# Kernel tuning notes

Hardware: AMD Instinct MI355X
Metric: run time of the kernel (lower is better)

The kernel has to match this reference:

```python
import jax, jax.numpy as jnp
import numpy as np

N_NODES = 50000
N_EDGES = 800000
IN_DIM = 128
HID_DIM = 128
OUT_DIM = 128


def setup_inputs() -> dict:
    key = jax.random.key(0)
    k = jax.random.split(key, 8)
    x = jax.random.normal(k[0], (N_NODES, IN_DIM), dtype=jnp.float32)
    edge_index = jax.random.randint(k[1], (2, N_EDGES), 0, N_NODES, dtype=jnp.int64)
    edge_weight = jax.random.uniform(k[2], (N_EDGES,), dtype=jnp.float32)
    # GCNConv params: weight [in, out] (glorot-ish), bias [out]
    W1 = jax.random.normal(k[3], (IN_DIM, HID_DIM), dtype=jnp.float32) / np.sqrt(IN_DIM)
    b1 = jnp.zeros((HID_DIM,), dtype=jnp.float32)
    W2 = jax.random.normal(k[4], (HID_DIM, OUT_DIM), dtype=jnp.float32) / np.sqrt(HID_DIM)
    b2 = jnp.zeros((OUT_DIM,), dtype=jnp.float32)
    return {"x": x, "edge_index": edge_index, "edge_weight": edge_weight,
            "W1": W1, "b1": b1, "W2": W2, "b2": b2}


def gcn_conv(x, W, b, src, dst, ew, n_nodes):
    """PyG GCNConv: add self-loops (weight 1), symmetric D^-1/2 (A+I) D^-1/2 norm."""
    h = x @ W  # [N, out]
    deg = jax.ops.segment_sum(ew, dst, num_segments=n_nodes) + 1.0  # +1 for self loop
    dis = jnp.where(deg > 0, jax.lax.rsqrt(deg), 0.0)  # deg^{-1/2}
    norm = dis[src] * ew * dis[dst]  # [E]
    msg = h[src] * norm[:, None]  # gather + weight -> [E, out]
    agg = jax.ops.segment_sum(msg, dst, num_segments=n_nodes)
    # self-loop contribution: norm_ii = dis[i] * 1 * dis[i]
    agg = agg + h * (dis * dis)[:, None]
    return agg + b


def reference(x, edge_index, edge_weight, W1, b1, W2, b2):
    src, dst = edge_index[0], edge_index[1]
    n = x.shape[0]
    h = gcn_conv(x, W1, b1, src, dst, edge_weight, n)
    h = jax.nn.relu(h)
    out = gcn_conv(h, W2, b2, src, dst, edge_weight, n)
    return out
```

## Files before the change

kernel.cpp:

```cpp
#include <hip/hip_runtime.h>

#define NDIM 128
#define NPART 8

typedef __attribute__((ext_vector_type(8))) short bf16x8;
typedef __attribute__((ext_vector_type(4))) float floatx4;

__device__ __forceinline__ float bflo(unsigned v){ return __uint_as_float(v << 16); }
__device__ __forceinline__ float bfhi(unsigned v){ return __uint_as_float(v & 0xffff0000u); }
__device__ __forceinline__ unsigned f2bf(float f){
  unsigned u = __float_as_uint(f);
  return (u + 0x7fffu + ((u >> 16) & 1u)) >> 16;
}

__global__ void k_prep0(unsigned long long* __restrict__ pk,
                        const float* __restrict__ W1, const float* __restrict__ W2,
                        unsigned short* __restrict__ Wp1, unsigned short* __restrict__ Wp2,
                        int n){
  int i = blockIdx.x * 256 + threadIdx.x;
  if (i < n) pk[i] = 0ULL;
  if (i < NDIM * NDIM){
    int k = i >> 7, c = i & 127;
    int kt = k >> 5, kq = (k >> 3) & 3, j = k & 7;
    int Lb = kq * 16 + (c & 15);
    int idx = (((kt * 8 + (c >> 4)) * 64) + Lb) * 8 + j;
    Wp1[idx] = (unsigned short)f2bf(W1[i]);
    Wp2[idx] = (unsigned short)f2bf(W2[i]);
  }
}

__global__ void k_deg(const int* __restrict__ ei, const float* __restrict__ ew,
                      unsigned long long* pk, unsigned short* __restrict__ rank, int E){
  int e = blockIdx.x * blockDim.x + threadIdx.x;
  if (e >= E) return;
  int d = ei[E + e];
  unsigned fx = (unsigned)__float2uint_rn(ew[e] * 1048576.0f);
  unsigned long long old = atomicAdd(&pk[d], (1ULL << 44) | (unsigned long long)fx);
  rank[e] = (unsigned short)(old >> 44);
}

__global__ __launch_bounds__(1024) void k_scan1(const unsigned long long* __restrict__ pk,
                                                int* __restrict__ off,
                                                int* __restrict__ bsum, int n){
  __shared__ int wsum[16];
  int t = threadIdx.x;
  int i = blockIdx.x * 1024 + t;
  int c = (i < n) ? (int)(pk[i] >> 44) : 0;
  int lane = t & 63, w = t >> 6;
  int v = c;
  #pragma unroll
  for (int d = 1; d < 64; d <<= 1){ int u = __shfl_up(v, d); if (lane >= d) v += u; }
  if (lane == 63) wsum[w] = v;
  __syncthreads();
  if (w == 0){
    int sv = (lane < 16) ? wsum[lane] : 0;
    #pragma unroll
    for (int d = 1; d < 16; d <<= 1){ int u = __shfl_up(sv, d); if (lane >= d) sv += u; }
    if (lane < 16) wsum[lane] = sv;
  }
  __syncthreads();
  int base = (w > 0) ? wsum[w - 1] : 0;
  if (i < n) off[i] = base + v - c;
  if (t == 1023) bsum[blockIdx.x] = wsum[15];
}

__global__ __launch_bounds__(1024) void k_scan23(int* __restrict__ off,
                                                 const int* __restrict__ bsum,
                                                 const unsigned long long* __restrict__ pk,
                                                 float* __restrict__ dis, int n, int E, int nb){
  __shared__ int sBase;
  int t = threadIdx.x;
  if (t < 64){
    int c2 = (t < nb) ? bsum[t] : 0;
    int v2 = c2;
    #pragma unroll
    for (int d = 1; d < 64; d <<= 1){ int u = __shfl_up(v2, d); if (t >= d) v2 += u; }
    if (t == (int)blockIdx.x) sBase = v2 - c2;
  }
  __syncthreads();
  int i = blockIdx.x * 1024 + t;
  if (i == 0) off[n] = E;
  if (i >= n) return;
  off[i] += sBase;
  float deg = 1.0f + (float)(pk[i] & ((1ULL << 44) - 1)) * (1.0f / 1048576.0f);
  dis[i] = rsqrtf(deg);
}

__global__ __launch_bounds__(256) void k_place(const int* __restrict__ ei,
                                               const float* __restrict__ ew,
                                               const unsigned short* __restrict__ rank,
                                               const float* __restrict__ dis,
                                               const int* __restrict__ off,
                                               unsigned* __restrict__ edges,
                                               int E, int N){
  int pid = blockIdx.x % NPART;
  int cid = blockIdx.x / NPART;
  int C   = gridDim.x / NPART;
  int per = (E + C - 1) / C;
  int e0 = cid * per;
  int e1 = min(e0 + per, E);
  int lo = (int)(((long long)pid * N) / NPART);
  int hi = (int)(((long long)(pid + 1) * N) / NPART);
  for (int e = e0 + threadIdx.x; e < e1; e += 256){
    int d = ei[E + e];
    if (d < lo || d >= hi) continue;
    int s = ei[e];
    float w = ew[e];
    int p = off[d] + (int)rank[e];
    edges[p] = (f2bf(dis[s] * w * dis[d]) << 16) | (unsigned)s;
  }
}

template<int XF32>
__global__ __launch_bounds__(256) void k_gemm_mfma(const void* __restrict__ Xv,
                                                   const unsigned short* __restrict__ Wp,
                                                   unsigned short* __restrict__ Hout,
                                                   int ntiles){
  __shared__ unsigned short Wb[4 * 8 * 64 * 8];
  int tid = threadIdx.x;
  for (int t = tid; t < 2048; t += 256)
    ((uint4*)Wb)[t] = ((const uint4*)Wp)[t];
  __syncthreads();

  int w = tid >> 6, L = tid & 63;
  int m = L & 15, q = L >> 4;
  for (int tile = blockIdx.x * 4 + w; tile < ntiles; tile += gridDim.x * 4){
    size_t row = (size_t)tile * 16 + m;
    floatx4 acc[8] = {};
    #pragma unroll
    for (int kt = 0; kt < 4; ++kt){
      bf16x8 a;
      if (XF32){
        const float* xp = (const float*)Xv + row * NDIM + kt * 32 + q * 8;
        float4 a0 = *(const float4*)xp;
        float4 a1 = *(const float4*)(xp + 4);
        unsigned short* as = (unsigned short*)&a;
        as[0] = f2bf(a0.x); as[1] = f2bf(a0.y); as[2] = f2bf(a0.z); as[3] = f2bf(a0.w);
        as[4] = f2bf(a1.x); as[5] = f2bf(a1.y); as[6] = f2bf(a1.z); as[7] = f2bf(a1.w);
      } else {
        a = *(const bf16x8*)((const unsigned short*)Xv + row * NDIM + kt * 32 + q * 8);
      }
      #pragma unroll
      for (int ct = 0; ct < 8; ++ct){
        bf16x8 b = *(const bf16x8*)&Wb[((kt * 8 + ct) * 64 + L) * 8];
        acc[ct] = __builtin_amdgcn_mfma_f32_16x16x32_bf16(a, b, acc[ct], 0, 0, 0);
      }
    }
    #pragma unroll
    for (int ct = 0; ct < 8; ++ct){
      #pragma unroll
      for (int r = 0; r < 4; ++r){
        size_t orow = (size_t)tile * 16 + q * 4 + r;
        Hout[orow * NDIM + ct * 16 + m] = (unsigned short)f2bf(acc[ct][r]);
      }
    }
  }
}

template<int OUT_F32>
__global__ __launch_bounds__(256) void k_agg(const unsigned short* __restrict__ H,
                                             const int* __restrict__ off,
                                             const unsigned* __restrict__ edges,
                                             const float* __restrict__ dis,
                                             const float* __restrict__ bias,
                                             void* __restrict__ out,
                                             int n, int do_relu){
  int g = threadIdx.x >> 6, L = threadIdx.x & 63;
  int i = blockIdx.x * 4 + g;
  if (i >= n) return;
  float di = dis[i];
  float dii = di * di;
  float2 bv = ((const float2*)bias)[L];
  unsigned hv = ((const unsigned*)(H + (size_t)i * NDIM))[L];
  float acc0 = fmaf(bflo(hv), dii, bv.x);
  float acc1 = fmaf(bfhi(hv), dii, bv.y);
  int p  = __builtin_amdgcn_readfirstlane(off[i]);
  int p1 = __builtin_amdgcn_readfirstlane(off[i + 1]);
  const char* Hb = (const char*)H;
  unsigned L4 = (unsigned)L * 4u;

  while (p + 16 <= p1){
    unsigned e[16], h[16];
    #pragma unroll
    for (int j = 0; j < 16; ++j) e[j] = __builtin_amdgcn_readfirstlane(edges[p + j]);
    #pragma unroll
    for (int j = 0; j < 16; ++j)
      h[j] = *(const unsigned*)(Hb + (((size_t)(e[j] & 0xFFFFu)) << 8) + L4);
    #pragma unroll
    for (int j = 0; j < 16; ++j){
      float w = bfhi(e[j]);
      acc0 = fmaf(bflo(h[j]), w, acc0);
      acc1 = fmaf(bfhi(h[j]), w, acc1);
    }
    p += 16;
  }
  if (p + 8 <= p1){
    unsigned e[8], h[8];
    #pragma unroll
    for (int j = 0; j < 8; ++j) e[j] = __builtin_amdgcn_readfirstlane(edges[p + j]);
    #pragma unroll
    for (int j = 0; j < 8; ++j)
      h[j] = *(const unsigned*)(Hb + (((size_t)(e[j] & 0xFFFFu)) << 8) + L4);
    #pragma unroll
    for (int j = 0; j < 8; ++j){
      float w = bfhi(e[j]);
      acc0 = fmaf(bflo(h[j]), w, acc0);
      acc1 = fmaf(bfhi(h[j]), w, acc1);
    }
    p += 8;
  }
  if (p + 4 <= p1){
    unsigned e[4], h[4];
    #pragma unroll
    for (int j = 0; j < 4; ++j) e[j] = __builtin_amdgcn_readfirstlane(edges[p + j]);
    #pragma unroll
    for (int j = 0; j < 4; ++j)
      h[j] = *(const unsigned*)(Hb + (((size_t)(e[j] & 0xFFFFu)) << 8) + L4);
    #pragma unroll
    for (int j = 0; j < 4; ++j){
      float w = bfhi(e[j]);
      acc0 = fmaf(bflo(h[j]), w, acc0);
      acc1 = fmaf(bfhi(h[j]), w, acc1);
    }
    p += 4;
  }
  for (; p < p1; ++p){
    unsigned e = __builtin_amdgcn_readfirstlane(edges[p]);
    unsigned h2 = *(const unsigned*)(Hb + (((size_t)(e & 0xFFFFu)) << 8) + L4);
    float w = bfhi(e);
    acc0 = fmaf(bflo(h2), w, acc0);
    acc1 = fmaf(bfhi(h2), w, acc1);
  }
  if (do_relu){ acc0 = fmaxf(acc0, 0.f); acc1 = fmaxf(acc1, 0.f); }
  if (OUT_F32){
    ((float2*)((float*)out + (size_t)i * NDIM))[L] = make_float2(acc0, acc1);
  } else {
    ((unsigned*)((unsigned short*)out + (size_t)i * NDIM))[L] = (f2bf(acc1) << 16) | f2bf(acc0);
  }
}

extern "C" void kernel_launch(void* const* d_in, const int* in_sizes, int n_in,
                              void* d_out, int out_size, void* d_ws, size_t ws_size,
                              hipStream_t stream){
  const float* x  = (const float*)d_in[0];
  const int*   ei = (const int*)  d_in[1];
  const float* ew = (const float*)d_in[2];
  const float* W1 = (const float*)d_in[3];
  const float* b1 = (const float*)d_in[4];
  const float* W2 = (const float*)d_in[5];
  const float* b2 = (const float*)d_in[6];
  float* out = (float*)d_out;
  int N = in_sizes[0] / NDIM;
  int E = in_sizes[2];
  int nb = (N + 1023) / 1024;
  int ntiles = N / 16;

  char* p = (char*)d_ws;
  auto alloc = [&](size_t b) -> char* { char* r = p; p += (b + 255) & ~(size_t)255; return r; };
  unsigned long long* pk = (unsigned long long*)alloc((size_t)N * 8);
  float*    dis   = (float*)   alloc((size_t)N * 4);
  int*      off   = (int*)     alloc((size_t)(N + 1) * 4);
  int*      bsum  = (int*)     alloc((size_t)64 * 4);
  unsigned short* rank = (unsigned short*)alloc((size_t)E * 2);
  unsigned short* Wp1 = (unsigned short*)alloc(NDIM * NDIM * 2);
  unsigned short* Wp2 = (unsigned short*)alloc(NDIM * NDIM * 2);
  unsigned* edges = (unsigned*)alloc((size_t)E * 4);
  unsigned short* R  = (unsigned short*)alloc((size_t)N * NDIM * 2);
  unsigned short* H2 = (unsigned short*)alloc((size_t)N * NDIM * 2);
  unsigned short* H1 = (unsigned short*)d_out;

  k_prep0<<<(N + 255) / 256, 256, 0, stream>>>(pk, W1, W2, Wp1, Wp2, N);
  k_deg  <<<(E + 255) / 256, 256, 0, stream>>>(ei, ew, pk, rank, E);
  k_scan1<<<nb, 1024, 0, stream>>>(pk, off, bsum, N);
  k_scan23<<<nb, 1024, 0, stream>>>(off, bsum, pk, dis, N, E, nb);
  k_place<<<NPART * 256, 256, 0, stream>>>(ei, ew, rank, dis, off, edges, E, N);

  int gg = (ntiles + 3) / 4;
  k_gemm_mfma<1><<<gg, 256, 0, stream>>>(x, Wp1, H1, ntiles);
  k_agg<0> <<<(N + 3) / 4, 256, 0, stream>>>(H1, off, edges, dis, b1, R, N, 1);
  k_gemm_mfma<0><<<gg, 256, 0, stream>>>(R, Wp2, H2, ntiles);
  k_agg<1> <<<(N + 3) / 4, 256, 0, stream>>>(H2, off, edges, dis, b2, out, N, 0);
}
```

Before: 228.4 us.

## Partition degree atomics by destination range and place edges via cursor atomics

The degree-count kernel now uses the same destination-partitioned grid as the placement kernel, so each block only issues atomics to nodes in one eighth of the range, which should improve L2 locality of the atomics. The per-edge rank array is removed. Placement now gets slots from atomicAdd on a cursor array initialised from the offsets. This trades the rank write and read for a second pass of atomics, and the order of edges within a node's segment becomes nondeterministic.

```diff
diff --git a/kernel.cpp b/kernel.cpp
--- a/kernel.cpp
+++ b/kernel.cpp
@@ -29,14 +29,23 @@
   }
 }
 
-__global__ void k_deg(const int* __restrict__ ei, const float* __restrict__ ew,
-                      unsigned long long* pk, unsigned short* __restrict__ rank, int E){
-  int e = blockIdx.x * blockDim.x + threadIdx.x;
-  if (e >= E) return;
-  int d = ei[E + e];
-  unsigned fx = (unsigned)__float2uint_rn(ew[e] * 1048576.0f);
-  unsigned long long old = atomicAdd(&pk[d], (1ULL << 44) | (unsigned long long)fx);
-  rank[e] = (unsigned short)(old >> 44);
+__global__ __launch_bounds__(256) void k_deg(const int* __restrict__ ei,
+                                             const float* __restrict__ ew,
+                                             unsigned long long* pk, int E, int N){
+  int pid = blockIdx.x % NPART;
+  int cid = blockIdx.x / NPART;
+  int C   = gridDim.x / NPART;
+  int per = (E + C - 1) / C;
+  int e0 = cid * per;
+  int e1 = min(e0 + per, E);
+  int lo = (int)(((long long)pid * N) / NPART);
+  int hi = (int)(((long long)(pid + 1) * N) / NPART);
+  for (int e = e0 + threadIdx.x; e < e1; e += 256){
+    int d = ei[E + e];
+    if (d < lo || d >= hi) continue;
+    unsigned fx = (unsigned)__float2uint_rn(ew[e] * 1048576.0f);
+    atomicAdd(&pk[d], (1ULL << 44) | (unsigned long long)fx);
+  }
 }
 
 __global__ __launch_bounds__(1024) void k_scan1(const unsigned long long* __restrict__ pk,
@@ -64,7 +73,7 @@
   if (t == 1023) bsum[blockIdx.x] = wsum[15];
 }
 
-__global__ __launch_bounds__(1024) void k_scan23(int* __restrict__ off,
+__global__ __launch_bounds__(1024) void k_scan23(int* __restrict__ off, int* __restrict__ cur,
                                                  const int* __restrict__ bsum,
                                                  const unsigned long long* __restrict__ pk,
                                                  float* __restrict__ dis, int n, int E, int nb){
@@ -81,16 +90,16 @@
   int i = blockIdx.x * 1024 + t;
   if (i == 0) off[n] = E;
   if (i >= n) return;
-  off[i] += sBase;
+  int o = off[i] + sBase;
+  off[i] = o; cur[i] = o;
   float deg = 1.0f + (float)(pk[i] & ((1ULL << 44) - 1)) * (1.0f / 1048576.0f);
   dis[i] = rsqrtf(deg);
 }
 
 __global__ __launch_bounds__(256) void k_place(const int* __restrict__ ei,
                                                const float* __restrict__ ew,
-                                               const unsigned short* __restrict__ rank,
                                                const float* __restrict__ dis,
-                                               const int* __restrict__ off,
+                                               int* __restrict__ cur,
                                                unsigned* __restrict__ edges,
                                                int E, int N){
   int pid = blockIdx.x % NPART;
@@ -106,7 +115,7 @@
     if (d < lo || d >= hi) continue;
     int s = ei[e];
     float w = ew[e];
-    int p = off[d] + (int)rank[e];
+    int p = atomicAdd(&cur[d], 1);
     edges[p] = (f2bf(dis[s] * w * dis[d]) << 16) | (unsigned)s;
   }
 }
@@ -259,9 +268,9 @@
   auto alloc = [&](size_t b) -> char* { char* r = p; p += (b + 255) & ~(size_t)255; return r; };
   unsigned long long* pk = (unsigned long long*)alloc((size_t)N * 8);
   float*    dis   = (float*)   alloc((size_t)N * 4);
+  int*      cur   = (int*)     alloc((size_t)N * 4);
   int*      off   = (int*)     alloc((size_t)(N + 1) * 4);
   int*      bsum  = (int*)     alloc((size_t)64 * 4);
-  unsigned short* rank = (unsigned short*)alloc((size_t)E * 2);
   unsigned short* Wp1 = (unsigned short*)alloc(NDIM * NDIM * 2);
   unsigned short* Wp2 = (unsigned short*)alloc(NDIM * NDIM * 2);
   unsigned* edges = (unsigned*)alloc((size_t)E * 4);
@@ -270,10 +279,10 @@
   unsigned short* H1 = (unsigned short*)d_out;
 
   k_prep0<<<(N + 255) / 256, 256, 0, stream>>>(pk, W1, W2, Wp1, Wp2, N);
-  k_deg  <<<(E + 255) / 256, 256, 0, stream>>>(ei, ew, pk, rank, E);
+  k_deg  <<<NPART * 256, 256, 0, stream>>>(ei, ew, pk, E, N);
   k_scan1<<<nb, 1024, 0, stream>>>(pk, off, bsum, N);
-  k_scan23<<<nb, 1024, 0, stream>>>(off, bsum, pk, dis, N, E, nb);
-  k_place<<<NPART * 256, 256, 0, stream>>>(ei, ew, rank, dis, off, edges, E, N);
+  k_scan23<<<nb, 1024, 0, stream>>>(off, cur, bsum, pk, dis, N, E, nb);
+  k_place<<<NPART * 256, 256, 0, stream>>>(ei, ew, dis, cur, edges, E, N);
 
   int gg = (ntiles + 3) / 4;
   k_gemm_mfma<1><<<gg, 256, 0, stream>>>(x, Wp1, H1, ntiles);
```

Measured after the change: 246.1 us. 7.7% more time.
